# Performance work log

Hardware: AMD Instinct MI355X
Metric: run time of the kernel (lower is better)

## Reference

```python
import jax, jax.numpy as jnp
import numpy as np

B, CN, CC, D, V = 65536, 16, 16, 128, 65
EPS = 1e-05

def setup_inputs() -> dict:
    key = jax.random.key(0)
    ks = jax.random.split(key, 7)
    x_num = jax.random.normal(ks[0], (B, CN), dtype=jnp.float32)
    x_cat = jax.random.randint(ks[1], (B, CC), 0, V, dtype=jnp.int32)
    means = jax.random.normal(ks[2], (CN,), dtype=jnp.float32)
    stds = jax.random.uniform(ks[3], (CN,), dtype=jnp.float32, minval=0.5, maxval=2.0)
    lin_W = jax.random.normal(ks[4], (CN, D), dtype=jnp.float32) * 0.02  # Linear(1,D) weight per numeric attr
    lin_b = jax.random.normal(ks[5], (CN, D), dtype=jnp.float32) * 0.02
    emb = jax.random.normal(ks[6], (CC, V, D), dtype=jnp.float32) * 0.02  # stacked embedding tables
    return {"x_num": x_num, "means": means, "stds": stds, "lin_W": lin_W,
            "lin_b": lin_b, "emb": emb, "x_cat": x_cat}

def reference(x_num, means, stds, lin_W, lin_b, emb, x_cat):
    # numeric attrs: sigmoid((x - mean)/(std + eps)) -> Linear(1,D), summed over attrs
    z = jax.nn.sigmoid((x_num - means) / (stds + EPS))          # [B, CN]
    h = jnp.einsum('bi,id->bd', z, lin_W) + lin_b.sum(axis=0)   # [B, D]
    # categorical attrs: per-attr embedding lookup, summed over attrs
    gathered = emb[jnp.arange(emb.shape[0]), x_cat]             # [B, CC, D]
    return h + gathered.sum(axis=1)                              # [B, D]
```

## Files before the change

### kernel.cpp

```cpp
#include <hip/hip_runtime.h>


constexpr int CN = 16;
constexpr int CC = 16;
constexpr int D  = 128;
constexpr int V  = 65;
constexpr float EPS = 1e-5f;
constexpr int ROWS_PER_BLOCK = 8;

__global__ __launch_bounds__(256) void embed_att_kernel(
    const float* __restrict__ x_num,
    const float* __restrict__ means,
    const float* __restrict__ stds,
    const float* __restrict__ lin_W,
    const float* __restrict__ lin_b,
    const float* __restrict__ emb,
    const int*  __restrict__ x_cat,
    float* __restrict__ out)
{
    __shared__ float z_s[ROWS_PER_BLOCK][CN];
    __shared__ int   idx_s[ROWS_PER_BLOCK][CC];
    __shared__ float w_s[CN * D];
    __shared__ float bsum_s[D];

    const int tid  = threadIdx.x;
    const int row0 = blockIdx.x * ROWS_PER_BLOCK;

    {
        const float4* w4 = (const float4*)lin_W;
        ((float4*)w_s)[tid]       = w4[tid];
        ((float4*)w_s)[tid + 256] = w4[tid + 256];
    }

    if (tid < D) {
        float s = 0.f;
#pragma unroll
        for (int i = 0; i < CN; ++i) s += lin_b[i * D + tid];
        bsum_s[tid] = s;
    }

    if (tid < ROWS_PER_BLOCK * CN) {
        const int r = tid >> 4, a = tid & 15;
        const float x = x_num[row0 * CN + tid];
        const float m = means[a];
        const float s = stds[a];
        const float t = (x - m) / (s + EPS);
        const float e = __builtin_amdgcn_exp2f(t * -1.44269504088896340736f);
        z_s[r][a]   = 1.0f / (1.0f + e);
        idx_s[r][a] = x_cat[row0 * CC + tid];
    }
    __syncthreads();

    const int r   = tid >> 5;
    const int g   = tid & 31;
    const int row = row0 + r;

    float acc[4];
    {
        const float4 b = ((const float4*)bsum_s)[g];
        acc[0] = b.x; acc[1] = b.y; acc[2] = b.z; acc[3] = b.w;
    }

#pragma unroll
    for (int i = 0; i < CN; ++i) {
        const float zi = z_s[r][i];
        const float4 w = ((const float4*)w_s)[i * 32 + g];
        acc[0] += zi * w.x; acc[1] += zi * w.y;
        acc[2] += zi * w.z; acc[3] += zi * w.w;
    }

#pragma unroll
    for (int c = 0; c < CC; ++c) {
        const int idx = idx_s[r][c];
        const float4 e = *(const float4*)&emb[(c * V + idx) * D + g * 4];
        acc[0] += e.x; acc[1] += e.y; acc[2] += e.z; acc[3] += e.w;
    }

    float4 o; o.x = acc[0]; o.y = acc[1]; o.z = acc[2]; o.w = acc[3];
    *(float4*)&out[row * D + g * 4] = o;
}

extern "C" void kernel_launch(void* const* d_in, const int* in_sizes, int n_in,
                              void* d_out, int out_size, void* d_ws, size_t ws_size,
                              hipStream_t stream) {
    const float* x_num = (const float*)d_in[0];
    const float* means = (const float*)d_in[1];
    const float* stds  = (const float*)d_in[2];
    const float* lin_W = (const float*)d_in[3];
    const float* lin_b = (const float*)d_in[4];
    const float* emb   = (const float*)d_in[5];
    const int*   x_cat = (const int*)d_in[6];
    float* out = (float*)d_out;

    const int nrows = in_sizes[0] / CN;
    const int grid  = nrows / ROWS_PER_BLOCK;

    embed_att_kernel<<<grid, 256, 0, stream>>>(x_num, means, stds, lin_W, lin_b,
                                               emb, x_cat, out);
}
```

Before: 99.12 us.

## Process 32 rows per block with register-resident weights and bias sums

Each block now handles 32 rows in four iterations instead of 8 rows. Each thread keeps its 16 lin_W float4 slices and the summed bias in registers, replacing the shared-memory weight copy and bias reduction. The z and index preprocessing is vectorized so all 256 threads take part. This spreads the per-block weight and bias loads over four times as many rows. In exchange, register pressure rises (64 floats for the weights) and the grid has four times fewer blocks.

```diff
diff --git a/kernel.cpp b/kernel.cpp
--- a/kernel.cpp
+++ b/kernel.cpp
@@ -6,7 +6,8 @@
 constexpr int D  = 128;
 constexpr int V  = 65;
 constexpr float EPS = 1e-5f;
-constexpr int ROWS_PER_BLOCK = 8;
+constexpr int TILE  = 32;
+constexpr int ITERS = 4;
 
 __global__ __launch_bounds__(256) void embed_att_kernel(
     const float* __restrict__ x_num,
@@ -18,66 +19,82 @@
     const int*  __restrict__ x_cat,
     float* __restrict__ out)
 {
-    __shared__ float z_s[ROWS_PER_BLOCK][CN];
-    __shared__ int   idx_s[ROWS_PER_BLOCK][CC];
-    __shared__ float w_s[CN * D];
-    __shared__ float bsum_s[D];
+    __shared__ float z_s[TILE * CN];
+    __shared__ int   idx_s[TILE * CC];
 
     const int tid  = threadIdx.x;
-    const int row0 = blockIdx.x * ROWS_PER_BLOCK;
+    const int row0 = blockIdx.x * TILE;
 
     {
-        const float4* w4 = (const float4*)lin_W;
-        ((float4*)w_s)[tid]       = w4[tid];
-        ((float4*)w_s)[tid + 256] = w4[tid + 256];
+        const float2 x2 = ((const float2*)(x_num + row0 * CN))[tid];
+        const int a0 = (tid & 7) * 2;
+        const float2 m2 = *(const float2*)&means[a0];
+        const float2 s2 = *(const float2*)&stds[a0];
+        float2 z2;
+        {
+            const float t0 = (x2.x - m2.x) / (s2.x + EPS);
+            const float e0 = __builtin_amdgcn_exp2f(t0 * -1.44269504088896340736f);
+            z2.x = 1.0f / (1.0f + e0);
+            const float t1 = (x2.y - m2.y) / (s2.y + EPS);
+            const float e1 = __builtin_amdgcn_exp2f(t1 * -1.44269504088896340736f);
+            z2.y = 1.0f / (1.0f + e1);
+        }
+        ((float2*)z_s)[tid]   = z2;
+        ((int2*)idx_s)[tid]   = ((const int2*)(x_cat + row0 * CC))[tid];
     }
 
-    if (tid < D) {
-        float s = 0.f;
+    const int g = tid & 31;
+    float4 wq[CN];
+    float bs0 = 0.f, bs1 = 0.f, bs2 = 0.f, bs3 = 0.f;
 #pragma unroll
-        for (int i = 0; i < CN; ++i) s += lin_b[i * D + tid];
-        bsum_s[tid] = s;
+    for (int i = 0; i < CN; ++i) {
+        wq[i] = *(const float4*)&lin_W[i * D + g * 4];
+        const float4 b = *(const float4*)&lin_b[i * D + g * 4];
+        bs0 += b.x; bs1 += b.y; bs2 += b.z; bs3 += b.w;
     }
 
-    if (tid < ROWS_PER_BLOCK * CN) {
-        const int r = tid >> 4, a = tid & 15;
-        const float x = x_num[row0 * CN + tid];
-        const float m = means[a];
-        const float s = stds[a];
-        const float t = (x - m) / (s + EPS);
-        const float e = __builtin_amdgcn_exp2f(t * -1.44269504088896340736f);
-        z_s[r][a]   = 1.0f / (1.0f + e);
-        idx_s[r][a] = x_cat[row0 * CC + tid];
-    }
     __syncthreads();
 
-    const int r   = tid >> 5;
-    const int g   = tid & 31;
-    const int row = row0 + r;
+    const int wv   = tid >> 6;
+    const int half = (tid >> 5) & 1;
+    const float* __restrict__ embg = emb + g * 4;
 
-    float acc[4];
-    {
-        const float4 b = ((const float4*)bsum_s)[g];
-        acc[0] = b.x; acc[1] = b.y; acc[2] = b.z; acc[3] = b.w;
-    }
+#pragma unroll 1
+    for (int t = 0; t < ITERS; ++t) {
+        const int r   = t * 8 + wv * 2 + half;
+        const int row = row0 + r;
+
+        const float4* zr = (const float4*)&z_s[r * CN];
+        const int4*   ir = (const int4*)&idx_s[r * CC];
+
+        float acc0 = bs0, acc1 = bs1, acc2 = bs2, acc3 = bs3;
 
 #pragma unroll
-    for (int i = 0; i < CN; ++i) {
-        const float zi = z_s[r][i];
-        const float4 w = ((const float4*)w_s)[i * 32 + g];
-        acc[0] += zi * w.x; acc[1] += zi * w.y;
-        acc[2] += zi * w.z; acc[3] += zi * w.w;
-    }
+        for (int k = 0; k < 4; ++k) {
+            const float4 z4 = zr[k];
+            float4 w;
+            w = wq[4*k+0]; acc0 += z4.x*w.x; acc1 += z4.x*w.y; acc2 += z4.x*w.z; acc3 += z4.x*w.w;
+            w = wq[4*k+1]; acc0 += z4.y*w.x; acc1 += z4.y*w.y; acc2 += z4.y*w.z; acc3 += z4.y*w.w;
+            w = wq[4*k+2]; acc0 += z4.z*w.x; acc1 += z4.z*w.y; acc2 += z4.z*w.z; acc3 += z4.z*w.w;
+            w = wq[4*k+3]; acc0 += z4.w*w.x; acc1 += z4.w*w.y; acc2 += z4.w*w.z; acc3 += z4.w*w.w;
+        }
 
 #pragma unroll
-    for (int c = 0; c < CC; ++c) {
-        const int idx = idx_s[r][c];
-        const float4 e = *(const float4*)&emb[(c * V + idx) * D + g * 4];
-        acc[0] += e.x; acc[1] += e.y; acc[2] += e.z; acc[3] += e.w;
+        for (int k = 0; k < 4; ++k) {
+            const int4 q = ir[k];
+            const float4 e0 = *(const float4*)&embg[((4*k+0)*V + q.x) * D];
+            const float4 e1 = *(const float4*)&embg[((4*k+1)*V + q.y) * D];
+            const float4 e2 = *(const float4*)&embg[((4*k+2)*V + q.z) * D];
+            const float4 e3 = *(const float4*)&embg[((4*k+3)*V + q.w) * D];
+            acc0 += e0.x; acc1 += e0.y; acc2 += e0.z; acc3 += e0.w;
+            acc0 += e1.x; acc1 += e1.y; acc2 += e1.z; acc3 += e1.w;
+            acc0 += e2.x; acc1 += e2.y; acc2 += e2.z; acc3 += e2.w;
+            acc0 += e3.x; acc1 += e3.y; acc2 += e3.z; acc3 += e3.w;
+        }
+
+        float4 o; o.x = acc0; o.y = acc1; o.z = acc2; o.w = acc3;
+        *(float4*)&out[row * D + g * 4] = o;
     }
-
-    float4 o; o.x = acc[0]; o.y = acc[1]; o.z = acc[2]; o.w = acc[3];
-    *(float4*)&out[row * D + g * 4] = o;
 }
 
 extern "C" void kernel_launch(void* const* d_in, const int* in_sizes, int n_in,
@@ -93,7 +110,7 @@
     float* out = (float*)d_out;
 
     const int nrows = in_sizes[0] / CN;
-    const int grid  = nrows / ROWS_PER_BLOCK;
+    const int grid  = nrows / TILE;
 
     embed_att_kernel<<<grid, 256, 0, stream>>>(x_num, means, stds, lin_W, lin_b,
                                                emb, x_cat, out);
```

Result: slower. 103.4 us (+4.3%).
